# Kernel optimization log

Measured on AMD Instinct MI355X. Metric: run time of the kernel, lower is better.

## Reference

```python
import jax, jax.numpy as jnp
import numpy as np

S = 1            # support_num
NEIGHBOR = 32    # neighbor_num for ball query
EPS = 1e-12

def _gather(t, idx):
    # t: (bs, N, C), idx: (bs, M, n) -> (bs, M, n, C)
    return jax.vmap(lambda tb, ib: tb[ib])(t, idx)

def _pick(t, idx):
    # t: (bs, M, C), idx: (bs, V) -> (bs, V, C)
    return jax.vmap(lambda tb, ib: tb[ib])(t, idx)

def _normalize(x, axis):
    return x / jnp.maximum(jnp.linalg.norm(x, axis=axis, keepdims=True), EPS)

def query_ball_point(radius, nsample, xyz, new_xyz):
    # PointNet++-style ball query: indices of first nsample points within radius,
    # missing slots filled with the first valid neighbor (self, since dist=0).
    sq = jnp.sum((new_xyz[:, :, None, :] - xyz[:, None, :, :]) ** 2, axis=-1)  # (bs,S,N)
    N = xyz.shape[1]
    idx = jnp.broadcast_to(jnp.arange(N), sq.shape)
    idx = jnp.where(sq > radius * radius, N, idx)
    idx = jnp.sort(idx, axis=-1)[:, :, :nsample]
    return jnp.where(idx == N, idx[:, :, :1], idx)

def _dir_norm(vertices, nbr_idx):
    nbrs = _gather(vertices, nbr_idx)                       # (bs,v,n,3)
    return _normalize(nbrs - vertices[:, :, None, :], axis=-1)

def conv_surface(nbr_idx, vertices, directions, K=32):
    # directions: (3, S*K)
    dn = _dir_norm(vertices, nbr_idx)
    theta = jax.nn.relu(jnp.einsum('bvnd,dk->bvnk', dn, _normalize(directions, 0)))
    bs, v, n, _ = theta.shape
    return theta.reshape(bs, v, n, S, K).max(axis=2).sum(axis=2)  # (bs,v,K)

def conv_layer(nbr_idx, vertices, fm, w, b, d, K=32):
    # w: (Cin,(S+1)*K), b: ((S+1)*K,), d: (3,S*K)
    dn = _dir_norm(vertices, nbr_idx)
    theta = jax.nn.relu(jnp.einsum('bvnd,dk->bvnk', dn, _normalize(d, 0)))  # (bs,v,n,S*K)
    f = jnp.einsum('bvc,ck->bvk', fm, w) + b                # (bs,v,(S+1)*K)
    center, support = f[..., :K], f[..., K:]
    sup = _gather(support, nbr_idx)                          # (bs,v,n,S*K)
    bs, v, n, _ = sup.shape
    act = (theta * sup).reshape(bs, v, n, S, K).max(axis=2).sum(axis=2)
    return center + act

def pool_layer(vertices, fm, radius, key, rate=4, nn_num=4):
    idx = query_ball_point(radius, nn_num, vertices, vertices)
    pooled = _gather(fm, idx).max(axis=2)                    # neighborhood max-pool
    v = vertices.shape[1]
    perm = jax.random.permutation(key, v)[: v // rate]       # random subsample (fixed key)
    return vertices[:, perm], pooled[:, perm]

def get_nearest_index(target, source):
    sq = jnp.sum((target[:, :, None, :] - source[:, None, :, :]) ** 2, axis=-1)
    return jnp.argmin(sq, axis=-1)                           # (bs, V_target)

def _forward(vertices, onehot, d0, w1, b1, dd1, w2, b2, dd2, w3, b3, dd3,
             w4, b4, dd4, w5, b5, dd5, w6, b6, dd6, w7, b7, dd7,
             cw1, cb1, cw2, cb2, cw3, cb3):
    relu = jax.nn.relu
    bs, V, _ = vertices.shape
    ni = query_ball_point(0.25, NEIGHBOR, vertices, vertices)
    fm0 = relu(conv_surface(ni, vertices, d0))
    fm1 = jnp.concatenate([fm0, relu(conv_layer(ni, vertices, fm0, w1, b1, dd1))], -1)
    fm2 = jnp.concatenate([fm1, relu(conv_layer(ni, vertices, fm1, w2, b2, dd2))], -1)
    v1, fp1 = pool_layer(vertices, fm2, 0.25, jax.random.fold_in(jax.random.key(42), 1))
    ni = query_ball_point(0.39, NEIGHBOR, v1, v1)
    fm3 = jnp.concatenate([fp1, relu(conv_layer(ni, v1, fp1, w3, b3, dd3))], -1)
    fm4 = jnp.concatenate([fm3, relu(conv_layer(ni, v1, fm3, w4, b4, dd4))], -1)
    fm5 = jnp.concatenate([fm4, relu(conv_layer(ni, v1, fm4, w5, b5, dd5))], -1)
    v2, fp2 = pool_layer(v1, fm5, 0.39, jax.random.fold_in(jax.random.key(42), 2))
    ni = query_ball_point(0.63, NEIGHBOR, v2, v2)
    fm6 = jnp.concatenate([fp2, relu(conv_layer(ni, v2, fp2, w6, b6, dd6))], -1)
    fm7 = jnp.concatenate([fm6, relu(conv_layer(ni, v2, fm6, w7, b7, dd7))], -1)
    f_global = fm7.max(axis=1)                               # (bs, 256)
    n1 = get_nearest_index(vertices, v1)
    n2 = get_nearest_index(vertices, v2)
    fuse = jnp.concatenate([
        fm0, fm1, fm2,
        _pick(fm3, n1), _pick(fm4, n1), _pick(fm5, n1),
        _pick(fm6, n2), _pick(fm7, n2),
        jnp.broadcast_to(f_global[:, None, :], (bs, V, f_global.shape[-1])),
        jnp.broadcast_to(onehot[:, None, :], (bs, V, onehot.shape[-1])),
    ], axis=-1)                                              # (bs, V, 1424)
    h = relu(jnp.einsum('bvc,oc->bvo', fuse, cw1) + cb1)
    h = relu(jnp.einsum('bvc,oc->bvo', h, cw2) + cb2)
    return jnp.einsum('bvc,oc->bvo', h, cw3) + cb3           # (bs, V, class_num)


def setup_inputs() -> dict:
    key = jax.random.key(0)
    ks = iter(jax.random.split(key, 40))
    bs, N, cat = 8, 2048, 16
    vertices = jax.random.uniform(next(ks), (bs, N, 3), dtype=jnp.float32)
    labels = jax.random.randint(next(ks), (bs,), 0, cat)
    onehot = jax.nn.one_hot(labels, cat, dtype=jnp.float32)
    def p(shape):
        return jax.random.normal(next(ks), shape, dtype=jnp.float32) * 0.05
    inp = {"vertices": vertices, "onehot": onehot, "d0": p((3, S * 32))}
    ins = [32, 64, 96, 128, 160, 192, 224]
    for i, c in enumerate(ins, start=1):
        inp[f"w{i}"] = p((c, (S + 1) * 32))
        inp[f"b{i}"] = p(((S + 1) * 32,))
        inp[f"dd{i}"] = p((3, S * 32))
    inp["cw1"] = p((1024, 1424)); inp["cb1"] = p((1024,))
    inp["cw2"] = p((512, 1024)); inp["cb2"] = p((512,))
    inp["cw3"] = p((50, 512)); inp["cb3"] = p((50,))
    return inp


def reference(vertices, onehot, d0, w1, b1, dd1, w2, b2, dd2, w3, b3, dd3,
              w4, b4, dd4, w5, b5, dd5, w6, b6, dd6, w7, b7, dd7,
              cw1, cb1, cw2, cb2, cw3, cb3):
    return _forward(vertices, onehot, d0, w1, b1, dd1, w2, b2, dd2, w3, b3, dd3,
                    w4, b4, dd4, w5, b5, dd5, w6, b6, dd6, w7, b7, dd7,
                    cw1, cb1, cw2, cb2, cw3, cb3)
```

## Files before the change

### kernel.cpp

```cpp
#include <hip/hip_runtime.h>
#include <hip/hip_bf16.h>

#define BS 8
#define V0 2048
#define V1N 512
#define V2N 128

typedef unsigned short ushort_t;
typedef __attribute__((ext_vector_type(8))) short bf16x8;
typedef __attribute__((ext_vector_type(4))) float f32x4;

__device__ __forceinline__ void tf2x32(unsigned k0, unsigned k1,
                                       unsigned x0, unsigned x1,
                                       unsigned &o0, unsigned &o1) {
  unsigned ks2 = k0 ^ k1 ^ 0x1BD11BDAu;
  x0 += k0; x1 += k1;
#define RR(r) { x0 += x1; x1 = (x1 << (r)) | (x1 >> (32 - (r))); x1 ^= x0; }
  RR(13) RR(15) RR(26) RR(6)   x0 += k1;  x1 += ks2 + 1u;
  RR(17) RR(29) RR(16) RR(24)  x0 += ks2; x1 += k0 + 2u;
  RR(13) RR(15) RR(26) RR(6)   x0 += k0;  x1 += k1 + 3u;
  RR(17) RR(29) RR(16) RR(24)  x0 += k1;  x1 += ks2 + 4u;
  RR(13) RR(15) RR(26) RR(6)   x0 += ks2; x1 += k0 + 5u;
#undef RR
  o0 = x0; o1 = x1;
}

__device__ __forceinline__ ushort_t f2bf(float f) {
  unsigned u = __float_as_uint(f);
  u += 0x7FFFu + ((u >> 16) & 1u);
  return (ushort_t)(u >> 16);
}

__device__ __forceinline__ float sqdist_f32(float cx, float cy, float cz,
                                            const float* p) {
  float dx = __fsub_rn(cx, p[0]);
  float dy = __fsub_rn(cy, p[1]);
  float dz = __fsub_rn(cz, p[2]);
  return __fadd_rn(__fadd_rn(__fmul_rn(dx, dx), __fmul_rn(dy, dy)),
                   __fmul_rn(dz, dz));
}

#define KP1 1472

#define PREP_BLKS 1025
#define QBP1_BLKS 512
__global__ __launch_bounds__(256) void misc1_kernel(
    int* __restrict__ rank, const float* __restrict__ cw1,
    const float* __restrict__ cw2, const float* __restrict__ cw3,
    const float* __restrict__ cb3, ushort_t* __restrict__ cw1b,
    ushort_t* __restrict__ cw2b, ushort_t* __restrict__ cw3b,
    float* __restrict__ cb3p, const float* __restrict__ pts,
    int* __restrict__ ni1) {
  int bid = blockIdx.x, tid = threadIdx.x;
  if (bid < 18) {
    __shared__ unsigned sb[2048];
    int seg, segfirst, n, base;
    if (bid < 8)       { seg = 0; segfirst = 0;  n = 2048; base = 0; }
    else if (bid < 16) { seg = 1; segfirst = 8;  n = 2048; base = 2048; }
    else               { seg = 2; segfirst = 16; n = 512;  base = 4096; }
    unsigned k0, k1, nk0, nk1, sk0, sk1;
    if (seg == 0) {
      tf2x32(0u, 42u, 0u, 1u, k0, k1);
      tf2x32(k0, k1, 0u, 1u, sk0, sk1);
    } else if (seg == 1) {
      tf2x32(0u, 42u, 0u, 1u, k0, k1);
      tf2x32(k0, k1, 0u, 0u, nk0, nk1);
      tf2x32(nk0, nk1, 0u, 1u, sk0, sk1);
    } else {
      tf2x32(0u, 42u, 0u, 2u, k0, k1);
      tf2x32(k0, k1, 0u, 1u, sk0, sk1);
    }
    for (int i = tid; i < n; i += 256) {
      unsigned o0, o1;
      tf2x32(sk0, sk1, 0u, (unsigned)i, o0, o1);
      sb[i] = o0 ^ o1;
    }
    __syncthreads();
    int tt = (bid - segfirst) * 256 + tid;
    unsigned bt = sb[tt];
    int cnt = 0;
#pragma unroll 8
    for (int s = 0; s < n; ++s) {
      unsigned bs = sb[s];
      cnt += (bs < bt) || (bs == bt && s < tt);
    }
    rank[base + tt] = cnt;
  } else if (bid < 18 + PREP_BLKS) {
    int c = (bid - 18) * 256 + tid;
    const int C1 = 1024 * (KP1 / 8);
    const int C2 = (512 * 1024) / 8;
    const int C3 = (128 * 512) / 8;
    if (c < C1) {
      int n = c / (KP1 / 8);
      int cc = c - n * (KP1 / 8);
      int k = cc * 8;
      bf16x8 o = (bf16x8){0, 0, 0, 0, 0, 0, 0, 0};
      if (k < 1424) {
        const float* src = cw1 + (size_t)n * 1424 + k;
        float4 lo = *(const float4*)src;
        float4 hi = *(const float4*)(src + 4);
        o[0] = (short)f2bf(lo.x); o[1] = (short)f2bf(lo.y);
        o[2] = (short)f2bf(lo.z); o[3] = (short)f2bf(lo.w);
        o[4] = (short)f2bf(hi.x); o[5] = (short)f2bf(hi.y);
        o[6] = (short)f2bf(hi.z); o[7] = (short)f2bf(hi.w);
      }
      *(bf16x8*)(cw1b + (size_t)c * 8) = o;
    } else if (c < C1 + C2) {
      int u = (c - C1) * 8;
      const float* src = cw2 + u;
      float4 lo = *(const float4*)src;
      float4 hi = *(const float4*)(src + 4);
      bf16x8 o;
      o[0] = (short)f2bf(lo.x); o[1] = (short)f2bf(lo.y);
      o[2] = (short)f2bf(lo.z); o[3] = (short)f2bf(lo.w);
      o[4] = (short)f2bf(hi.x); o[5] = (short)f2bf(hi.y);
      o[6] = (short)f2bf(hi.z); o[7] = (short)f2bf(hi.w);
      *(bf16x8*)(cw2b + u) = o;
    } else if (c < C1 + C2 + C3) {
      int u = (c - C1 - C2) * 8;
      int n = u >> 9, k = u & 511;
      bf16x8 o = (bf16x8){0, 0, 0, 0, 0, 0, 0, 0};
      if (n < 50) {
        const float* src = cw3 + (size_t)n * 512 + k;
        float4 lo = *(const float4*)src;
        float4 hi = *(const float4*)(src + 4);
        o[0] = (short)f2bf(lo.x); o[1] = (short)f2bf(lo.y);
        o[2] = (short)f2bf(lo.z); o[3] = (short)f2bf(lo.w);
        o[4] = (short)f2bf(hi.x); o[5] = (short)f2bf(hi.y);
        o[6] = (short)f2bf(hi.z); o[7] = (short)f2bf(hi.w);
      }
      *(bf16x8*)(cw3b + u) = o;
    } else if (c < C1 + C2 + C3 + 16) {
      int u = (c - C1 - C2 - C3) * 8;
#pragma unroll
      for (int e = 0; e < 8; ++e)
        cb3p[u + e] = (u + e) < 50 ? cb3[u + e] : 0.f;
    }
  } else {
    __shared__ float spts[V0 * 3];
    int bq = bid - 18 - PREP_BLKS;
    int qbase = bq * 32;
    int b = qbase >> 11;
    const float* base = pts + (size_t)b * V0 * 3;
    for (int i = tid; i < V0 * 3 / 4; i += 256)
      ((float4*)spts)[i] = ((const float4*)base)[i];
    __syncthreads();
    int lane = tid & 63, wv = tid >> 6;
    for (int rep = 0; rep < 8; ++rep) {
      int qoff = wv * 8 + rep;
      int qi = (qbase & 2047) + qoff;
      int wid = qbase + qoff;
      float cx = spts[qi * 3], cy = spts[qi * 3 + 1], cz = spts[qi * 3 + 2];
      int cnt = 0, idx0 = 0;
      for (int j0 = 0; j0 < V0; j0 += 64) {
        int j = j0 + lane;
        float d2 = sqdist_f32(cx, cy, cz, spts + (size_t)j * 3);
        bool in = (d2 <= 0.0625f);
        unsigned long long mask = __ballot(in);
        if (cnt == 0 && mask) idx0 = j0 + __builtin_ctzll(mask);
        if (in) {
          int rk = cnt + __popcll(mask & ((1ull << lane) - 1ull));
          if (rk < 32) ni1[(size_t)wid * 32 + rk] = j;
        }
        cnt += __popcll(mask);
        if (cnt >= 32) break;
      }
      for (int s = cnt + lane; s < 32; s += 64) ni1[(size_t)wid * 32 + s] = idx0;
    }
  }
}

__device__ __forceinline__ void dirn(const float* base, int v, int nb,
                                     float& ox, float& oy, float& oz) {
  float dx = __fsub_rn(base[nb * 3 + 0], base[v * 3 + 0]);
  float dy = __fsub_rn(base[nb * 3 + 1], base[v * 3 + 1]);
  float dz = __fsub_rn(base[nb * 3 + 2], base[v * 3 + 2]);
  float s2 = __fadd_rn(__fadd_rn(__fmul_rn(dx, dx), __fmul_rn(dy, dy)),
                       __fmul_rn(dz, dz));
  float nrm = fmaxf(__fsqrt_rn(s2), 1e-12f);
  ox = __fdiv_rn(dx, nrm); oy = __fdiv_rn(dy, nrm); oz = __fdiv_rn(dz, nrm);
}

__device__ __forceinline__ void norm_col(const float* d, int k,
                                         float& ox, float& oy, float& oz) {
  float x = d[k], y = d[32 + k], z = d[64 + k];
  float s2 = __fadd_rn(__fadd_rn(__fmul_rn(x, x), __fmul_rn(y, y)),
                       __fmul_rn(z, z));
  float nrm = fmaxf(__fsqrt_rn(s2), 1e-12f);
  ox = __fdiv_rn(x, nrm); oy = __fdiv_rn(y, nrm); oz = __fdiv_rn(z, nrm);
}

__global__ __launch_bounds__(256) void misc2_kernel(
    const int* __restrict__ rank, int* __restrict__ perm1,
    int* __restrict__ perm2, const float* __restrict__ pts,
    const int* __restrict__ ni, const float* __restrict__ d0,
    const float* __restrict__ w1, const float* __restrict__ b1,
    float* __restrict__ out, float* __restrict__ fn) {
  int bid = blockIdx.x, tid = threadIdx.x;
  if (bid == 0) {
    __shared__ int a1[2048];
    __shared__ int a2[2048];
    for (int i = tid; i < 2048; i += 256) a1[rank[i]] = i;
    __syncthreads();
    for (int i = tid; i < 2048; i += 256) a2[rank[2048 + i]] = a1[i];
    __syncthreads();
    for (int i = tid; i < 512; i += 256) perm1[i] = a2[i];
    for (int i = tid; i < 512; i += 256) a1[rank[4096 + i]] = i;
    __syncthreads();
    for (int i = tid; i < 128; i += 256) perm2[i] = a1[i];
    return;
  }
  __shared__ float sdir[3][32];
  __shared__ float sdn[8][32][3];
  __shared__ float sfm[8][32];
  if (tid < 32) {
    float x, y, z; norm_col(d0, tid, x, y, z);
    sdir[0][tid] = x; sdir[1][tid] = y; sdir[2][tid] = z;
  }
  int vloc = tid >> 5, k = tid & 31;
  size_t bvg = (size_t)(bid - 1) * 8 + vloc;
  int b = (int)(bvg >> 11), v = (int)(bvg & 2047);
  const float* base = pts + (size_t)b * V0 * 3;
  int nb = ni[bvg * 32 + k];
  float x, y, z; dirn(base, v, nb, x, y, z);
  sdn[vloc][k][0] = x; sdn[vloc][k][1] = y; sdn[vloc][k][2] = z;
  __syncthreads();
  float m = 0.f;
  for (int n = 0; n < 32; ++n) {
    float d = sdn[vloc][n][0] * sdir[0][k] + sdn[vloc][n][1] * sdir[1][k] +
              sdn[vloc][n][2] * sdir[2][k];
    m = fmaxf(m, fmaxf(d, 0.f));
  }
  out[bvg * 96 + k] = m;
  sfm[vloc][k] = m;
  __syncthreads();
  float a1v = b1[k], a2v = b1[k + 32];
  for (int c = 0; c < 32; ++c) {
    float vv = sfm[vloc][c];
    a1v += vv * w1[c * 64 + k];
    a2v += vv * w1[c * 64 + k + 32];
  }
  fn[bvg * 64 + k] = a1v;
  fn[bvg * 64 + k + 32] = a2v;
}

__global__ __launch_bounds__(256) void conv_act_kernel(
    const float* __restrict__ pts, const float* __restrict__ dd,
    const int* __restrict__ ni, const float* __restrict__ f,
    float* __restrict__ out, int Nv, int ldout, int colofs,
    const float* __restrict__ wn, const float* __restrict__ bn,
    float* __restrict__ fn) {
  __shared__ float sdir[3][32];
  __shared__ float sdn[8][32][3];
  __shared__ int sidx[8][32];
  __shared__ float sfm[8][256];
  int tid = threadIdx.x;
  if (tid < 32) {
    float x, y, z; norm_col(dd, tid, x, y, z);
    sdir[0][tid] = x; sdir[1][tid] = y; sdir[2][tid] = z;
  }
  int vloc = tid >> 5, k = tid & 31;
  size_t bvg = (size_t)blockIdx.x * 8 + vloc;
  int b = (int)(bvg / Nv), v = (int)(bvg % Nv);
  const float* base = pts + (size_t)b * Nv * 3;
  int nb = ni[bvg * 32 + k];
  float x, y, z; dirn(base, v, nb, x, y, z);
  sdn[vloc][k][0] = x; sdn[vloc][k][1] = y; sdn[vloc][k][2] = z;
  sidx[vloc][k] = nb;
  __syncthreads();
  float m = -INFINITY;
  size_t fb = (size_t)b * Nv * 64;
  for (int n = 0; n < 32; ++n) {
    float th = fmaxf(sdn[vloc][n][0] * sdir[0][k] + sdn[vloc][n][1] * sdir[1][k] +
                     sdn[vloc][n][2] * sdir[2][k], 0.f);
    float sup = f[fb + (size_t)sidx[vloc][n] * 64 + 32 + k];
    m = fmaxf(m, th * sup);
  }
  float center = f[bvg * 64 + k];
  float res = fmaxf(center + m, 0.f);
  out[bvg * ldout + colofs + k] = res;
  if (wn) {
    size_t rowbase = (size_t)blockIdx.x * 8;
#pragma unroll 1
    for (int r = 0; r < 8; ++r)
      if (tid < colofs) sfm[r][tid] = out[(rowbase + r) * ldout + tid];
    sfm[vloc][colofs + k] = res;
    __syncthreads();
    int cin = colofs + 32;
    float a1v = bn[k], a2v = bn[k + 32];
    for (int c = 0; c < cin; ++c) {
      float vv = sfm[vloc][c];
      a1v += vv * wn[c * 64 + k];
      a2v += vv * wn[c * 64 + k + 32];
    }
    fn[bvg * 64 + k] = a1v;
    fn[bvg * 64 + k + 32] = a2v;
  }
}

__global__ __launch_bounds__(256) void conv_act_qbp_kernel(
    const float* __restrict__ pts, int Nv, float rrq,
    const float* __restrict__ dd, int* __restrict__ ni_out,
    const float* __restrict__ f, float* __restrict__ out, int ldout,
    int colofs, const float* __restrict__ wn, const float* __restrict__ bn,
    float* __restrict__ fn) {
  __shared__ float spts[512 * 3];
  __shared__ float sdir[3][32];
  __shared__ float sdn[8][32][3];
  __shared__ int sni[8][32];
  __shared__ float sfm[8][256];
  int tid = threadIdx.x;
  int b = (blockIdx.x * 8) / Nv;
  int vbase = (blockIdx.x * 8) % Nv;
  const float* gp = pts + (size_t)b * Nv * 3;
  for (int i = tid; i < Nv * 3; i += 256) spts[i] = gp[i];
  if (tid < 32) {
    float x, y, z; norm_col(dd, tid, x, y, z);
    sdir[0][tid] = x; sdir[1][tid] = y; sdir[2][tid] = z;
  }
  __syncthreads();
  int lane = tid & 63, wv = tid >> 6;
  for (int rep = 0; rep < 2; ++rep) {
    int vl = wv * 2 + rep;
    int v = vbase + vl;
    float cx = spts[v * 3], cy = spts[v * 3 + 1], cz = spts[v * 3 + 2];
    int cnt = 0, idx0 = 0;
    for (int j0 = 0; j0 < Nv; j0 += 64) {
      int j = j0 + lane;
      float d2 = sqdist_f32(cx, cy, cz, spts + (size_t)j * 3);
      bool in = (d2 <= rrq);
      unsigned long long mask = __ballot(in);
      if (cnt == 0 && mask) idx0 = j0 + __builtin_ctzll(mask);
      if (in) {
        int rk = cnt + __popcll(mask & ((1ull << lane) - 1ull));
        if (rk < 32) sni[vl][rk] = j;
      }
      cnt += __popcll(mask);
      if (cnt >= 32) break;
    }
    for (int s = cnt + lane; s < 32; s += 64) sni[vl][s] = idx0;
  }
  __syncthreads();
  ni_out[(size_t)(blockIdx.x * 8) * 32 + tid] = sni[tid >> 5][tid & 31];
  int vloc = tid >> 5, k = tid & 31;
  size_t bvg = (size_t)blockIdx.x * 8 + vloc;
  int v = vbase + vloc;
  int nb = sni[vloc][k];
  float x, y, z; dirn(spts, v, nb, x, y, z);
  sdn[vloc][k][0] = x; sdn[vloc][k][1] = y; sdn[vloc][k][2] = z;
  __syncthreads();
  float m = -INFINITY;
  size_t fb = (size_t)b * Nv * 64;
  for (int n = 0; n < 32; ++n) {
    float th = fmaxf(sdn[vloc][n][0] * sdir[0][k] + sdn[vloc][n][1] * sdir[1][k] +
                     sdn[vloc][n][2] * sdir[2][k], 0.f);
    float sup = f[fb + (size_t)sni[vloc][n] * 64 + 32 + k];
    m = fmaxf(m, th * sup);
  }
  float center = f[bvg * 64 + k];
  float res = fmaxf(center + m, 0.f);
  out[bvg * ldout + colofs + k] = res;
  size_t rowbase = (size_t)blockIdx.x * 8;
#pragma unroll 1
  for (int r = 0; r < 8; ++r)
    if (tid < colofs) sfm[r][tid] = out[(rowbase + r) * ldout + tid];
  sfm[vloc][colofs + k] = res;
  __syncthreads();
  int cin = colofs + 32;
  float a1v = bn[k], a2v = bn[k + 32];
  for (int c = 0; c < cin; ++c) {
    float vv = sfm[vloc][c];
    a1v += vv * wn[c * 64 + k];
    a2v += vv * wn[c * 64 + k + 32];
  }
  fn[bvg * 64 + k] = a1v;
  fn[bvg * 64 + k + 32] = a2v;
}

__global__ __launch_bounds__(256) void pool_kernel(
    const float* __restrict__ pts_in, const float* __restrict__ fm_in,
    int ld_in, int C, int Nv_in, const int* __restrict__ perm, int Nv_out,
    float rr, float* __restrict__ pts_out, float* __restrict__ fm_out,
    int ld_out, const float* __restrict__ wn, const float* __restrict__ bn,
    float* __restrict__ fn) {
  __shared__ float spf[4][192];
  int wv = threadIdx.x >> 6;
  int lane = threadIdx.x & 63;
  int wid = blockIdx.x * 4 + wv;
  int b = wid / Nv_out, pp = wid - b * Nv_out;
  int v = perm[pp];
  const float* base = pts_in + (size_t)b * Nv_in * 3;
  float cx = base[v * 3], cy = base[v * 3 + 1], cz = base[v * 3 + 2];
  int nb[4]; int cnt = 0;
  for (int j0 = 0; j0 < Nv_in && cnt < 4; j0 += 64) {
    int j = j0 + lane;
    float d2 = sqdist_f32(cx, cy, cz, base + (size_t)j * 3);
    unsigned long long mask = __ballot(d2 <= rr);
    while (mask && cnt < 4) {
      int bp = __builtin_ctzll(mask);
      mask &= mask - 1;
      nb[cnt++] = j0 + bp;
    }
  }
  for (int q = cnt; q < 4; ++q) nb[q] = nb[0];
  if (lane < 3) pts_out[(size_t)wid * 3 + lane] = base[v * 3 + lane];
  size_t inrow = (size_t)b * Nv_in;
  size_t outrow = (size_t)wid * ld_out;
  for (int c = lane; c < C; c += 64) {
    float m = fm_in[(inrow + nb[0]) * ld_in + c];
    m = fmaxf(m, fm_in[(inrow + nb[1]) * ld_in + c]);
    m = fmaxf(m, fm_in[(inrow + nb[2]) * ld_in + c]);
    m = fmaxf(m, fm_in[(inrow + nb[3]) * ld_in + c]);
    fm_out[outrow + c] = m;
    spf[wv][c] = m;
  }
  __syncthreads();
  int o = threadIdx.x & 63, w_ = threadIdx.x >> 6;
  int wid0 = blockIdx.x * 4 + w_;
  float a = bn[o];
  for (int c = 0; c < C; ++c) a += spf[w_][c] * wn[c * 64 + o];
  fn[(size_t)wid0 * 64 + o] = a;
}

__global__ __launch_bounds__(256) void gmax_kernel(
    const float* __restrict__ fm, float* __restrict__ out) {
  __shared__ float red[8][32];
  int b = blockIdx.x >> 3, cg = blockIdx.x & 7;
  int vsub = threadIdx.x >> 5, cl = threadIdx.x & 31;
  int c = cg * 32 + cl;
  float m = -INFINITY;
  for (int v = vsub; v < V2N; v += 8)
    m = fmaxf(m, fm[((size_t)b * V2N + v) * 256 + c]);
  red[vsub][cl] = m;
  __syncthreads();
  if (vsub == 0) {
#pragma unroll
    for (int r = 1; r < 8; ++r) m = fmaxf(m, red[r][cl]);
    out[b * 256 + c] = m;
  }
}

__global__ __launch_bounds__(256) void fuse_row_kernel(
    const float* __restrict__ fm2, const float* __restrict__ fm5,
    const float* __restrict__ fm7, const float* __restrict__ fglob,
    const float* __restrict__ onehot, const float* __restrict__ verts,
    const float* __restrict__ v1, const float* __restrict__ v2,
    ushort_t* __restrict__ fuse_b) {
  __shared__ unsigned long long sred[8];
  __shared__ int sn12[2];
  int bv = blockIdx.x;
  int b = bv >> 11;
  int tid = threadIdx.x;
  int lane = tid & 63, wv = tid >> 6;
  float cx = verts[(size_t)bv * 3 + 0];
  float cy = verts[(size_t)bv * 3 + 1];
  float cz = verts[(size_t)bv * 3 + 2];
  unsigned long long b1 = ~0ull, b2 = ~0ull;
  const float* s1 = v1 + (size_t)b * V1N * 3;
  for (int j = tid; j < V1N; j += 256) {
    float d2 = sqdist_f32(cx, cy, cz, s1 + (size_t)j * 3);
    unsigned long long key =
        (((unsigned long long)__float_as_uint(d2)) << 32) | (unsigned)j;
    b1 = b1 < key ? b1 : key;
  }
  const float* s2 = v2 + (size_t)b * V2N * 3;
  if (tid < V2N) {
    float d2 = sqdist_f32(cx, cy, cz, s2 + (size_t)tid * 3);
    b2 = (((unsigned long long)__float_as_uint(d2)) << 32) | (unsigned)tid;
  }
#pragma unroll
  for (int off = 32; off > 0; off >>= 1) {
    unsigned long long o1 = __shfl_down(b1, off);
    unsigned long long o2 = __shfl_down(b2, off);
    b1 = b1 < o1 ? b1 : o1;
    b2 = b2 < o2 ? b2 : o2;
  }
  if (lane == 0) { sred[wv] = b1; sred[4 + wv] = b2; }
  __syncthreads();
  if (tid == 0) {
    unsigned long long m1 = sred[0], m2 = sred[4];
#pragma unroll
    for (int r = 1; r < 4; ++r) {
      m1 = m1 < sred[r] ? m1 : sred[r];
      m2 = m2 < sred[4 + r] ? m2 : sred[4 + r];
    }
    sn12[0] = (int)(m1 & 0xffffffffu);
    sn12[1] = (int)(m2 & 0xffffffffu);
  }
  __syncthreads();
  int sn1 = sn12[0], sn2 = sn12[1];
  const float* r2 = fm2 + (size_t)bv * 96;
  const float* r5 = fm5 + ((size_t)b * V1N + sn1) * 192;
  const float* r7 = fm7 + ((size_t)b * V2N + sn2) * 256;
  const float* rg = fglob + b * 256;
  const float* roh = onehot + b * 16;
  if (tid < KP1 / 8) {
    int c = tid * 8;
    const float* src = nullptr;
    if (c < 192) {
      int cc = (c < 32) ? c : (c < 96 ? c - 32 : c - 96);
      src = r2 + cc;
    } else if (c < 672) {
      int cc = (c < 320) ? c - 192 : (c < 480 ? c - 320 : c - 480);
      src = r5 + cc;
    } else if (c < 1152) {
      int cc = (c < 896) ? c - 672 : c - 896;
      src = r7 + cc;
    } else if (c < 1408) {
      src = rg + (c - 1152);
    } else if (c < 1424) {
      src = roh + (c - 1408);
    }
    float4 lo = make_float4(0.f, 0.f, 0.f, 0.f), hi = lo;
    if (src) { lo = *(const float4*)src; hi = *(const float4*)(src + 4); }
    bf16x8 o;
    o[0] = (short)f2bf(lo.x); o[1] = (short)f2bf(lo.y);
    o[2] = (short)f2bf(lo.z); o[3] = (short)f2bf(lo.w);
    o[4] = (short)f2bf(hi.x); o[5] = (short)f2bf(hi.y);
    o[6] = (short)f2bf(hi.z); o[7] = (short)f2bf(hi.w);
    *(bf16x8*)(fuse_b + (size_t)bv * KP1 + c) = o;
  }
}

typedef const __attribute__((address_space(1))) unsigned int gas_u32;
typedef __attribute__((address_space(3))) unsigned int las_u32;

__global__ __launch_bounds__(256) void gemm_mfma_nt(
    const ushort_t* __restrict__ A, const ushort_t* __restrict__ B,
    const float* __restrict__ bias, ushort_t* __restrict__ Cb,
    float* __restrict__ Cf, int K, int ldc, int nvalid, int mode) {
  __shared__ ushort_t As[128 * 64];
  __shared__ ushort_t Bs[128 * 64];
  int tid = threadIdx.x;
  int lane = tid & 63, w = tid >> 6;
  int wm = (w >> 1) * 64, wn = (w & 1) * 64;
  int nb = gridDim.x;
  int flat = blockIdx.x + nb * blockIdx.y;
  int xcd = flat & 7, slot = flat >> 3;
  int nidx = slot % nb;
  int mband = xcd + 8 * (slot / nb);
  int bm = mband * 128, bn = nidx * 128;
  f32x4 acc[4][4];
#pragma unroll
  for (int i = 0; i < 4; ++i)
#pragma unroll
    for (int j = 0; j < 4; ++j) acc[i][j] = (f32x4){0.f, 0.f, 0.f, 0.f};

  const ushort_t* gA[4];
  const ushort_t* gB[4];
  ushort_t* lA[4];
  ushort_t* lB[4];
  int rsub = lane >> 3;
  int scol = ((lane & 7) ^ rsub) * 8;
#pragma unroll
  for (int g = 0; g < 4; ++g) {
    int r = w * 32 + g * 8 + rsub;
    gA[g] = A + (size_t)(bm + r) * K + scol;
    gB[g] = B + (size_t)(bn + r) * K + scol;
    lA[g] = As + (w * 32 + g * 8) * 64;
    lB[g] = Bs + (w * 32 + g * 8) * 64;
  }
  int rA = lane & 15, q = lane >> 4;
  int r7 = rA & 7;

  for (int k0 = 0; k0 < K; k0 += 64) {
#pragma unroll
    for (int g = 0; g < 4; ++g)
      __builtin_amdgcn_global_load_lds((gas_u32*)(gA[g] + k0), (las_u32*)lA[g],
                                       16, 0, 0);
#pragma unroll
    for (int g = 0; g < 4; ++g)
      __builtin_amdgcn_global_load_lds((gas_u32*)(gB[g] + k0), (las_u32*)lB[g],
                                       16, 0, 0);
    __syncthreads();
#pragma unroll
    for (int s = 0; s < 2; ++s) {
      int pc = ((s * 4 + q) ^ r7) * 8;
      bf16x8 af[4], bfr[4];
#pragma unroll
      for (int i = 0; i < 4; ++i)
        af[i] = *(const bf16x8*)(As + (wm + i * 16 + rA) * 64 + pc);
#pragma unroll
      for (int j = 0; j < 4; ++j)
        bfr[j] = *(const bf16x8*)(Bs + (wn + j * 16 + rA) * 64 + pc);
#pragma unroll
      for (int i = 0; i < 4; ++i)
#pragma unroll
        for (int j = 0; j < 4; ++j)
          acc[i][j] = __builtin_amdgcn_mfma_f32_16x16x32_bf16(af[i], bfr[j],
                                                              acc[i][j], 0, 0, 0);
    }
    __syncthreads();
  }

  int rowq = (lane >> 4) * 4;
  int coll = lane & 15;
#pragma unroll
  for (int i = 0; i < 4; ++i) {
#pragma unroll
    for (int j = 0; j < 4; ++j) {
      int col = bn + wn + j * 16 + coll;
      float bi = bias[col];
#pragma unroll
      for (int r = 0; r < 4; ++r) {
        int row = bm + wm + i * 16 + rowq + r;
        float v = acc[i][j][r] + bi;
        if (mode == 0) {
          Cb[(size_t)row * ldc + col] = f2bf(fmaxf(v, 0.f));
        } else if (col < nvalid) {
          Cf[(size_t)row * ldc + col] = v;
        }
      }
    }
  }
}

__global__ __launch_bounds__(512, 2) void gemm256_mfma_nt(
    const ushort_t* __restrict__ A, const ushort_t* __restrict__ B,
    const float* __restrict__ bias, ushort_t* __restrict__ Cb,
    int K, int ldc) {
  __shared__ ushort_t As[2 * 256 * 64];
  __shared__ ushort_t Bs[2 * 256 * 64];
  int tid = threadIdx.x;
  int lane = tid & 63, w = tid >> 6;
  int wm = (w >> 2) * 128, wn = (w & 3) * 64;

  int flat = blockIdx.x;
  int xcd = flat & 7, slot = flat >> 3;
  int nidx = slot & 3, mband = xcd + 8 * (slot >> 2);
  int bm = mband * 256, bn = nidx * 256;

  f32x4 acc[8][4];
#pragma unroll
  for (int i = 0; i < 8; ++i)
#pragma unroll
    for (int j = 0; j < 4; ++j) acc[i][j] = (f32x4){0.f, 0.f, 0.f, 0.f};

  int rloc = tid >> 3, cch = tid & 7;
  int gc = (cch ^ (rloc & 7)) * 8;
  const ushort_t* gA[4];
  const ushort_t* gB[4];
#pragma unroll
  for (int i = 0; i < 4; ++i) {
    gA[i] = A + (size_t)(bm + i * 64 + rloc) * K + gc;
    gB[i] = B + (size_t)(bn + i * 64 + rloc) * K + gc;
  }
  int lofs = tid * 8;

  int rA = lane & 15, r7 = lane & 7;
  int qlane = lane >> 4;
  int pc0 = (qlane ^ r7) * 8;
  int pc1 = ((4 + qlane) ^ r7) * 8;

  int NT = K >> 6;

#pragma unroll
  for (int i = 0; i < 4; ++i) {
    __builtin_amdgcn_global_load_lds((gas_u32*)gA[i],
                                     (las_u32*)(As + i * 4096 + lofs), 16, 0, 0);
    gA[i] += 64;
  }
#pragma unroll
  for (int i = 0; i < 4; ++i) {
    __builtin_amdgcn_global_load_lds((gas_u32*)gB[i],
                                     (las_u32*)(Bs + i * 4096 + lofs), 16, 0, 0);
    gB[i] += 64;
  }

  for (int t = 0; t < NT; ++t) {
    int doff = (t & 1) * 16384;
    int poff = doff ^ 16384;
    const ushort_t* Ab = As + doff;
    const ushort_t* Bb = Bs + doff;
    bool pf = (t + 1 < NT);

    asm volatile("s_waitcnt vmcnt(0)" ::: "memory");
    __builtin_amdgcn_sched_barrier(0);
    __builtin_amdgcn_s_barrier();
    __builtin_amdgcn_sched_barrier(0);

#pragma unroll
    for (int q = 0; q < 4; ++q) {
      int band = q >> 1, kh = q & 1;
      int pck = kh ? pc1 : pc0;

      bf16x8 af[4], bfq[4];
#pragma unroll
      for (int fi = 0; fi < 4; ++fi)
        af[fi] = *(const bf16x8*)(Ab + (wm + band * 64 + fi * 16 + rA) * 64 + pck);
#pragma unroll
      for (int fj = 0; fj < 4; ++fj)
        bfq[fj] = *(const bf16x8*)(Bb + (wn + fj * 16 + rA) * 64 + pck);

      if (pf) {
        if (q < 2) {
          __builtin_amdgcn_global_load_lds(
              (gas_u32*)gA[2 * q],
              (las_u32*)(As + poff + (2 * q) * 4096 + lofs), 16, 0, 0);
          __builtin_amdgcn_global_load_lds(
              (gas_u32*)gA[2 * q + 1],
              (las_u32*)(As + poff + (2 * q + 1) * 4096 + lofs), 16, 0, 0);
          gA[2 * q] += 64;
          gA[2 * q + 1] += 64;
        } else {
          int i = 2 * (q - 2);
          __builtin_amdgcn_global_load_lds(
              (gas_u32*)gB[i],
              (las_u32*)(Bs + poff + i * 4096 + lofs), 16, 0, 0);
          __builtin_amdgcn_global_load_lds(
              (gas_u32*)gB[i + 1],
              (las_u32*)(Bs + poff + (i + 1) * 4096 + lofs), 16, 0, 0);
          gB[i] += 64;
          gB[i + 1] += 64;
        }
      }

      __builtin_amdgcn_sched_barrier(0);
      __builtin_amdgcn_s_barrier();
      asm volatile("s_waitcnt lgkmcnt(0)" ::: "memory");
      __builtin_amdgcn_sched_barrier(0);

      __builtin_amdgcn_s_setprio(1);
#pragma unroll
      for (int fi = 0; fi < 4; ++fi)
#pragma unroll
        for (int fj = 0; fj < 4; ++fj)
          acc[band * 4 + fi][fj] = __builtin_amdgcn_mfma_f32_16x16x32_bf16(
              af[fi], bfq[fj], acc[band * 4 + fi][fj], 0, 0, 0);
      __builtin_amdgcn_s_setprio(0);
      __builtin_amdgcn_sched_barrier(0);
      __builtin_amdgcn_s_barrier();
      __builtin_amdgcn_sched_barrier(0);
    }
  }

  int rowq = (lane >> 4) * 4;
  int coll = lane & 15;
  float bi[4];
#pragma unroll
  for (int j = 0; j < 4; ++j) bi[j] = bias[bn + wn + j * 16 + coll];
#pragma unroll
  for (int i = 0; i < 8; ++i) {
#pragma unroll
    for (int j = 0; j < 4; ++j) {
      int col = bn + wn + j * 16 + coll;
#pragma unroll
      for (int r = 0; r < 4; ++r) {
        int row = bm + wm + i * 16 + rowq + r;
        float v = acc[i][j][r] + bi[j];
        Cb[(size_t)row * ldc + col] = f2bf(fmaxf(v, 0.f));
      }
    }
  }
}

extern "C" void kernel_launch(void* const* d_in, const int* in_sizes, int n_in,
                              void* d_out, int out_size, void* d_ws,
                              size_t ws_size, hipStream_t stream) {
  const float* vertices = (const float*)d_in[0];
  const float* onehot = (const float*)d_in[1];
  const float* d0 = (const float*)d_in[2];
  const float *w[8], *bb[8], *dd[8];
  for (int i = 1; i <= 7; ++i) {
    w[i] = (const float*)d_in[3 * i];
    bb[i] = (const float*)d_in[3 * i + 1];
    dd[i] = (const float*)d_in[3 * i + 2];
  }
  const float* cw1 = (const float*)d_in[24];
  const float* cb1 = (const float*)d_in[25];
  const float* cw2 = (const float*)d_in[26];
  const float* cb2 = (const float*)d_in[27];
  const float* cw3 = (const float*)d_in[28];
  const float* cb3 = (const float*)d_in[29];
  float* out = (float*)d_out;

  char* wsp = (char*)d_ws;
  size_t off = 0;
  auto alloc = [&](size_t bytes) -> void* {
    void* p = wsp + off;
    off += (bytes + 255) & ~(size_t)255;
    return p;
  };
  const int M = BS * V0;
  int* rank = (int*)alloc(4608 * 4);
  int* perm1 = (int*)alloc(512 * 4);
  int* perm2 = (int*)alloc(128 * 4);
  int* ni1 = (int*)alloc((size_t)BS * V0 * 32 * 4);
  int* ni2 = (int*)alloc((size_t)BS * V1N * 32 * 4);
  int* ni3 = (int*)alloc((size_t)BS * V2N * 32 * 4);
  float* fm2buf = (float*)alloc((size_t)BS * V0 * 96 * 4);
  float* fm5buf = (float*)alloc((size_t)BS * V1N * 192 * 4);
  float* fm7buf = (float*)alloc((size_t)BS * V2N * 256 * 4);
  float* fbuf = (float*)alloc((size_t)BS * V0 * 64 * 4);
  float* v1 = (float*)alloc((size_t)BS * V1N * 3 * 4);
  float* v2 = (float*)alloc((size_t)BS * V2N * 3 * 4);
  float* fglob = (float*)alloc((size_t)BS * 256 * 4);
  ushort_t* fuse_b = (ushort_t*)alloc((size_t)M * KP1 * 2);
  ushort_t* h1b = (ushort_t*)alloc((size_t)M * 1024 * 2);
  ushort_t* h2b = (ushort_t*)alloc((size_t)M * 512 * 2);
  ushort_t* cw1b = (ushort_t*)alloc((size_t)1024 * KP1 * 2);
  ushort_t* cw2b = (ushort_t*)alloc((size_t)512 * 1024 * 2);
  ushort_t* cw3b = (ushort_t*)alloc((size_t)128 * 512 * 2);
  float* cb3p = (float*)alloc(128 * 4);

  float rr1 = 0.0625f;
  float rr2 = (float)(0.39 * 0.39);
  float rr3 = (float)(0.63 * 0.63);

  misc1_kernel<<<18 + PREP_BLKS + QBP1_BLKS, 256, 0, stream>>>(
      rank, cw1, cw2, cw3, cb3, cw1b, cw2b, cw3b, cb3p, vertices, ni1);
  misc2_kernel<<<1 + BS * V0 / 8, 256, 0, stream>>>(
      rank, perm1, perm2, vertices, ni1, d0, w[1], bb[1], fm2buf, fbuf);
  conv_act_kernel<<<BS * V0 / 8, 256, 0, stream>>>(
      vertices, dd[1], ni1, fbuf, fm2buf, V0, 96, 32, w[2], bb[2], fbuf);
  conv_act_kernel<<<BS * V0 / 8, 256, 0, stream>>>(
      vertices, dd[2], ni1, fbuf, fm2buf, V0, 96, 64, nullptr, nullptr, nullptr);
  pool_kernel<<<BS * V1N / 4, 256, 0, stream>>>(
      vertices, fm2buf, 96, 96, V0, perm1, V1N, rr1, v1, fm5buf, 192,
      w[3], bb[3], fbuf);
  conv_act_qbp_kernel<<<BS * V1N / 8, 256, 0, stream>>>(
      v1, V1N, rr2, dd[3], ni2, fbuf, fm5buf, 192, 96, w[4], bb[4], fbuf);
  conv_act_kernel<<<BS * V1N / 8, 256, 0, stream>>>(
      v1, dd[4], ni2, fbuf, fm5buf, V1N, 192, 128, w[5], bb[5], fbuf);
  conv_act_kernel<<<BS * V1N / 8, 256, 0, stream>>>(
      v1, dd[5], ni2, fbuf, fm5buf, V1N, 192, 160, nullptr, nullptr, nullptr);
  pool_kernel<<<BS * V2N / 4, 256, 0, stream>>>(
      v1, fm5buf, 192, 192, V1N, perm2, V2N, rr2, v2, fm7buf, 256,
      w[6], bb[6], fbuf);
  conv_act_qbp_kernel<<<BS * V2N / 8, 256, 0, stream>>>(
      v2, V2N, rr3, dd[6], ni3, fbuf, fm7buf, 256, 192, w[7], bb[7], fbuf);
  conv_act_kernel<<<BS * V2N / 8, 256, 0, stream>>>(
      v2, dd[7], ni3, fbuf, fm7buf, V2N, 256, 224, nullptr, nullptr, nullptr);
  gmax_kernel<<<64, 256, 0, stream>>>(fm7buf, fglob);
  fuse_row_kernel<<<M, 256, 0, stream>>>(fm2buf, fm5buf, fm7buf, fglob, onehot,
                                         vertices, v1, v2, fuse_b);
  gemm256_mfma_nt<<<(M / 256) * (1024 / 256), 512, 0, stream>>>(
      fuse_b, cw1b, cb1, h1b, KP1, 1024);
  gemm_mfma_nt<<<dim3(512 / 128, M / 128), 256, 0, stream>>>(
      h1b, cw2b, cb2, h2b, nullptr, 1024, 512, 512, 0);
  gemm_mfma_nt<<<dim3(1, M / 128), 256, 0, stream>>>(
      h2b, cw3b, cb3p, nullptr, out, 512, 50, 50, 1);
}
```

Measured before the change: 387.5 us.

## Move permutation ranking into misc2 and split perm inversion into own kernel

Moves the threefry-based random ranking blocks out of the first fused kernel into the second fused kernel, and moves the rank-to-permutation inversion into a new single-block kernel launched after it. This rebalances the work across launches so the slow O(n^2) ranking blocks run alongside the conv work instead of the weight conversion and ball query. It adds one extra kernel launch, and the single-block perm kernel sits on the critical path.

```diff
diff --git a/kernel.cpp b/kernel.cpp
--- a/kernel.cpp
+++ b/kernel.cpp
@@ -45,48 +45,14 @@
 #define PREP_BLKS 1025
 #define QBP1_BLKS 512
 __global__ __launch_bounds__(256) void misc1_kernel(
-    int* __restrict__ rank, const float* __restrict__ cw1,
-    const float* __restrict__ cw2, const float* __restrict__ cw3,
-    const float* __restrict__ cb3, ushort_t* __restrict__ cw1b,
-    ushort_t* __restrict__ cw2b, ushort_t* __restrict__ cw3b,
-    float* __restrict__ cb3p, const float* __restrict__ pts,
-    int* __restrict__ ni1) {
+    const float* __restrict__ cw1, const float* __restrict__ cw2,
+    const float* __restrict__ cw3, const float* __restrict__ cb3,
+    ushort_t* __restrict__ cw1b, ushort_t* __restrict__ cw2b,
+    ushort_t* __restrict__ cw3b, float* __restrict__ cb3p,
+    const float* __restrict__ pts, int* __restrict__ ni1) {
   int bid = blockIdx.x, tid = threadIdx.x;
-  if (bid < 18) {
-    __shared__ unsigned sb[2048];
-    int seg, segfirst, n, base;
-    if (bid < 8)       { seg = 0; segfirst = 0;  n = 2048; base = 0; }
-    else if (bid < 16) { seg = 1; segfirst = 8;  n = 2048; base = 2048; }
-    else               { seg = 2; segfirst = 16; n = 512;  base = 4096; }
-    unsigned k0, k1, nk0, nk1, sk0, sk1;
-    if (seg == 0) {
-      tf2x32(0u, 42u, 0u, 1u, k0, k1);
-      tf2x32(k0, k1, 0u, 1u, sk0, sk1);
-    } else if (seg == 1) {
-      tf2x32(0u, 42u, 0u, 1u, k0, k1);
-      tf2x32(k0, k1, 0u, 0u, nk0, nk1);
-      tf2x32(nk0, nk1, 0u, 1u, sk0, sk1);
-    } else {
-      tf2x32(0u, 42u, 0u, 2u, k0, k1);
-      tf2x32(k0, k1, 0u, 1u, sk0, sk1);
-    }
-    for (int i = tid; i < n; i += 256) {
-      unsigned o0, o1;
-      tf2x32(sk0, sk1, 0u, (unsigned)i, o0, o1);
-      sb[i] = o0 ^ o1;
-    }
-    __syncthreads();
-    int tt = (bid - segfirst) * 256 + tid;
-    unsigned bt = sb[tt];
-    int cnt = 0;
-#pragma unroll 8
-    for (int s = 0; s < n; ++s) {
-      unsigned bs = sb[s];
-      cnt += (bs < bt) || (bs == bt && s < tt);
-    }
-    rank[base + tt] = cnt;
-  } else if (bid < 18 + PREP_BLKS) {
-    int c = (bid - 18) * 256 + tid;
+  if (bid < PREP_BLKS) {
+    int c = bid * 256 + tid;
     const int C1 = 1024 * (KP1 / 8);
     const int C2 = (512 * 1024) / 8;
     const int C3 = (128 * 512) / 8;
@@ -138,7 +104,7 @@
     }
   } else {
     __shared__ float spts[V0 * 3];
-    int bq = bid - 18 - PREP_BLKS;
+    int bq = bid - PREP_BLKS;
     int qbase = bq * 32;
     int b = qbase >> 11;
     const float* base = pts + (size_t)b * V0 * 3;
@@ -191,23 +157,44 @@
 }
 
 __global__ __launch_bounds__(256) void misc2_kernel(
-    const int* __restrict__ rank, int* __restrict__ perm1,
-    int* __restrict__ perm2, const float* __restrict__ pts,
+    int* __restrict__ rank, const float* __restrict__ pts,
     const int* __restrict__ ni, const float* __restrict__ d0,
     const float* __restrict__ w1, const float* __restrict__ b1,
     float* __restrict__ out, float* __restrict__ fn) {
   int bid = blockIdx.x, tid = threadIdx.x;
-  if (bid == 0) {
-    __shared__ int a1[2048];
-    __shared__ int a2[2048];
-    for (int i = tid; i < 2048; i += 256) a1[rank[i]] = i;
+  if (bid < 18) {
+    __shared__ unsigned sb[2048];
+    int seg, segfirst, n, base;
+    if (bid < 8)       { seg = 0; segfirst = 0;  n = 2048; base = 0; }
+    else if (bid < 16) { seg = 1; segfirst = 8;  n = 2048; base = 2048; }
+    else               { seg = 2; segfirst = 16; n = 512;  base = 4096; }
+    unsigned k0, k1, nk0, nk1, sk0, sk1;
+    if (seg == 0) {
+      tf2x32(0u, 42u, 0u, 1u, k0, k1);
+      tf2x32(k0, k1, 0u, 1u, sk0, sk1);
+    } else if (seg == 1) {
+      tf2x32(0u, 42u, 0u, 1u, k0, k1);
+      tf2x32(k0, k1, 0u, 0u, nk0, nk1);
+      tf2x32(nk0, nk1, 0u, 1u, sk0, sk1);
+    } else {
+      tf2x32(0u, 42u, 0u, 2u, k0, k1);
+      tf2x32(k0, k1, 0u, 1u, sk0, sk1);
+    }
+    for (int i = tid; i < n; i += 256) {
+      unsigned o0, o1;
+      tf2x32(sk0, sk1, 0u, (unsigned)i, o0, o1);
+      sb[i] = o0 ^ o1;
+    }
     __syncthreads();
-    for (int i = tid; i < 2048; i += 256) a2[rank[2048 + i]] = a1[i];
-    __syncthreads();
-    for (int i = tid; i < 512; i += 256) perm1[i] = a2[i];
-    for (int i = tid; i < 512; i += 256) a1[rank[4096 + i]] = i;
-    __syncthreads();
-    for (int i = tid; i < 128; i += 256) perm2[i] = a1[i];
+    int tt = (bid - segfirst) * 256 + tid;
+    unsigned bt = sb[tt];
+    int cnt = 0;
+#pragma unroll 8
+    for (int s = 0; s < n; ++s) {
+      unsigned bs = sb[s];
+      cnt += (bs < bt) || (bs == bt && s < tt);
+    }
+    rank[base + tt] = cnt;
     return;
   }
   __shared__ float sdir[3][32];
@@ -218,7 +205,7 @@
     sdir[0][tid] = x; sdir[1][tid] = y; sdir[2][tid] = z;
   }
   int vloc = tid >> 5, k = tid & 31;
-  size_t bvg = (size_t)(bid - 1) * 8 + vloc;
+  size_t bvg = (size_t)(bid - 18) * 8 + vloc;
   int b = (int)(bvg >> 11), v = (int)(bvg & 2047);
   const float* base = pts + (size_t)b * V0 * 3;
   int nb = ni[bvg * 32 + k];
@@ -242,6 +229,22 @@
   }
   fn[bvg * 64 + k] = a1v;
   fn[bvg * 64 + k + 32] = a2v;
+}
+
+__global__ __launch_bounds__(256) void perm_kernel(
+    const int* __restrict__ rank, int* __restrict__ perm1,
+    int* __restrict__ perm2) {
+  int tid = threadIdx.x;
+  __shared__ int a1[2048];
+  __shared__ int a2[2048];
+  for (int i = tid; i < 2048; i += 256) a1[rank[i]] = i;
+  __syncthreads();
+  for (int i = tid; i < 2048; i += 256) a2[rank[2048 + i]] = a1[i];
+  __syncthreads();
+  for (int i = tid; i < 512; i += 256) perm1[i] = a2[i];
+  for (int i = tid; i < 512; i += 256) a1[rank[4096 + i]] = i;
+  __syncthreads();
+  for (int i = tid; i < 128; i += 256) perm2[i] = a1[i];
 }
 
 __global__ __launch_bounds__(256) void conv_act_kernel(
@@ -807,10 +810,11 @@
   float rr2 = (float)(0.39 * 0.39);
   float rr3 = (float)(0.63 * 0.63);
 
-  misc1_kernel<<<18 + PREP_BLKS + QBP1_BLKS, 256, 0, stream>>>(
-      rank, cw1, cw2, cw3, cb3, cw1b, cw2b, cw3b, cb3p, vertices, ni1);
-  misc2_kernel<<<1 + BS * V0 / 8, 256, 0, stream>>>(
-      rank, perm1, perm2, vertices, ni1, d0, w[1], bb[1], fm2buf, fbuf);
+  misc1_kernel<<<PREP_BLKS + QBP1_BLKS, 256, 0, stream>>>(
+      cw1, cw2, cw3, cb3, cw1b, cw2b, cw3b, cb3p, vertices, ni1);
+  misc2_kernel<<<18 + BS * V0 / 8, 256, 0, stream>>>(
+      rank, vertices, ni1, d0, w[1], bb[1], fm2buf, fbuf);
+  perm_kernel<<<1, 256, 0, stream>>>(rank, perm1, perm2);
   conv_act_kernel<<<BS * V0 / 8, 256, 0, stream>>>(
       vertices, dd[1], ni1, fbuf, fm2buf, V0, 96, 32, w[2], bb[2], fbuf);
   conv_act_kernel<<<BS * V0 / 8, 256, 0, stream>>>(
```

After: 414.7 us. 7.0% more time.
